# Kernel optimization log

Hardware: AMD Instinct MI355X
Metric: run time of the kernel (lower is better)

Reference implementation:

```python
import jax, jax.numpy as jnp
import numpy as np
import math

B, T, DIM = 2, 2048, 2048
N_HEADS, HEAD_DIM = 16, 128
SOFT_CAP = 30.0
EPS = 1e-6


def setup_inputs() -> dict:
    key = jax.random.key(0)
    ks = jax.random.split(key, 8)
    s = 0.02
    x = jax.random.normal(ks[0], (B, T, DIM), dtype=jnp.float32)
    # additive causal mask: 0 on/below diagonal, -1e9 above
    causal = jnp.tril(jnp.ones((T, T), dtype=bool))
    mask = jnp.where(causal, 0.0, -1e9).astype(jnp.float32)[None, None]
    Wq = jax.random.normal(ks[1], (DIM, DIM), dtype=jnp.float32) * s
    Wk = jax.random.normal(ks[2], (DIM, DIM), dtype=jnp.float32) * s
    Wv = jax.random.normal(ks[3], (DIM, DIM), dtype=jnp.float32) * s
    Wo = jax.random.normal(ks[4], (DIM, DIM), dtype=jnp.float32) * s
    ln_w = jnp.ones((DIM,), dtype=jnp.float32)
    gate_W = jax.random.normal(ks[5], (DIM, DIM), dtype=jnp.float32) * s
    gate_b = jnp.zeros((DIM,), dtype=jnp.float32)
    return {"x": x, "mask": mask, "Wq": Wq, "Wk": Wk, "Wv": Wv,
            "Wo": Wo, "ln_w": ln_w, "gate_W": gate_W, "gate_b": gate_b}


def reference(x, mask, Wq, Wk, Wv, Wo, ln_w, gate_W, gate_b):
    residual = x
    # RMSNorm
    xn = x * jax.lax.rsqrt(jnp.mean(x * x, axis=-1, keepdims=True) + EPS) * ln_w
    # projections (torch Linear: y = x @ W.T)
    q = (xn @ Wq.T).reshape(B, T, N_HEADS, HEAD_DIM)
    k = (xn @ Wk.T).reshape(B, T, N_HEADS, HEAD_DIM)
    v = (xn @ Wv.T).reshape(B, T, N_HEADS, HEAD_DIM)
    scale = 1.0 / math.sqrt(HEAD_DIM)
    logits = jnp.einsum('bqhd,bkhd->bhqk', q, k) * scale
    logits = SOFT_CAP * jnp.tanh(logits / SOFT_CAP)
    logits = logits + mask
    probs = jax.nn.softmax(logits, axis=-1)
    out = jnp.einsum('bhqk,bkhd->bqhd', probs, v).reshape(B, T, DIM)
    out = out @ Wo.T
    alpha = jax.nn.sigmoid(residual @ gate_W.T + gate_b)
    return (1.0 - alpha) * residual + alpha * out
```

## Files before the change

kernel.cpp:

```cpp
#include <hip/hip_runtime.h>
#include <hip/hip_bf16.h>
#include <cstdint>
#include <cstddef>

typedef __bf16 v8bf __attribute__((ext_vector_type(8)));
typedef float  v4f  __attribute__((ext_vector_type(4)));

using bf16 = __hip_bfloat16;

constexpr int Bdim  = 2;
constexpr int Tdim  = 2048;
constexpr int DIM   = 2048;
constexpr int NH    = 16;
constexpr int HD    = 128;
constexpr int Mrows = Bdim * Tdim;
constexpr size_t NEL  = (size_t)Mrows * DIM;
constexpr size_t W_EL = (size_t)DIM * DIM;

enum { MODE_PLAIN = 0, MODE_QK = 1, MODE_VT = 2, MODE_FINAL = 3 };

__device__ __forceinline__ float bf2f(bf16 v) { return __bfloat162float(v); }
__device__ __forceinline__ bf16  f2bf(float v) { return __float2bfloat16(v); }

__device__ __forceinline__ v8bf load8(const bf16* p) {
    return *reinterpret_cast<const v8bf*>(p);
}
__device__ __forceinline__ v8bf load8(const float* p) {
    const float4 a = *reinterpret_cast<const float4*>(p);
    const float4 b = *reinterpret_cast<const float4*>(p + 4);
    v8bf r;
    r[0] = (__bf16)a.x; r[1] = (__bf16)a.y; r[2] = (__bf16)a.z; r[3] = (__bf16)a.w;
    r[4] = (__bf16)b.x; r[5] = (__bf16)b.y; r[6] = (__bf16)b.z; r[7] = (__bf16)b.w;
    return r;
}

__device__ __forceinline__ void gll16(const void* g, void* l) {
    __builtin_amdgcn_global_load_lds(
        (__attribute__((address_space(1))) void*)g,
        (__attribute__((address_space(3))) void*)l, 16, 0, 0);
}

__global__ __launch_bounds__(256) void rms_xn_kernel(const float* __restrict__ x,
                                                     const float* __restrict__ lnw,
                                                     bf16* __restrict__ xn) {
    const int row  = blockIdx.x;
    const int base = threadIdx.x * 8;
    const float* xr = x + (size_t)row * DIM;

    const float4 a = *reinterpret_cast<const float4*>(xr + base);
    const float4 b = *reinterpret_cast<const float4*>(xr + base + 4);
    float ss = a.x*a.x + a.y*a.y + a.z*a.z + a.w*a.w
             + b.x*b.x + b.y*b.y + b.z*b.z + b.w*b.w;
#pragma unroll
    for (int off = 32; off >= 1; off >>= 1) ss += __shfl_xor(ss, off);

    __shared__ float red[4];
    const int wave = threadIdx.x >> 6;
    if ((threadIdx.x & 63) == 0) red[wave] = ss;
    __syncthreads();
    const float s = rsqrtf((red[0] + red[1] + red[2] + red[3]) * (1.0f / DIM) + 1e-6f);

    const float4 la = *reinterpret_cast<const float4*>(lnw + base);
    const float4 lb = *reinterpret_cast<const float4*>(lnw + base + 4);
    v8bf o;
    o[0] = (__bf16)(a.x * s * la.x); o[1] = (__bf16)(a.y * s * la.y);
    o[2] = (__bf16)(a.z * s * la.z); o[3] = (__bf16)(a.w * s * la.w);
    o[4] = (__bf16)(b.x * s * lb.x); o[5] = (__bf16)(b.y * s * lb.y);
    o[6] = (__bf16)(b.z * s * lb.z); o[7] = (__bf16)(b.w * s * lb.w);
    *reinterpret_cast<v8bf*>(xn + (size_t)row * DIM + base) = o;
}

__global__ __launch_bounds__(256) void conv_bf16_kernel(const float* __restrict__ s0,
                                                        const float* __restrict__ s1,
                                                        bf16* __restrict__ d0,
                                                        bf16* __restrict__ d1) {
    const int t = blockIdx.x >> 11;
    const float* s = t ? s1 : s0;
    bf16* d = t ? d1 : d0;
    const size_t i = (((size_t)(blockIdx.x & 2047)) * 256 + threadIdx.x) * 8;
    *reinterpret_cast<v8bf*>(d + i) = load8(s + i);
}

__global__ __launch_bounds__(256) void gemm_bt(
        const bf16* __restrict__ X0, const bf16* __restrict__ W0, bf16* __restrict__ Y0, int m0,
        const bf16* __restrict__ X1, const bf16* __restrict__ W1, bf16* __restrict__ Y1, int m1,
        const bf16* __restrict__ X2, const bf16* __restrict__ W2, bf16* __restrict__ Y2, int m2,
        float* __restrict__ Yf, const bf16* __restrict__ O2,
        const float* __restrict__ XR, const float* __restrict__ bias) {
    constexpr int BM = 128, BK = 32;
    __shared__ __align__(16) bf16 As[BM * BK];
    __shared__ __align__(16) bf16 Bs[BM * BK];

    const int sel = blockIdx.x >> 4;
    const bf16* X; const bf16* W; bf16* Y; int mode;
    if (sel == 0)      { X = X0; W = W0; Y = Y0; mode = m0; }
    else if (sel == 1) { X = X1; W = W1; Y = Y1; mode = m1; }
    else               { X = X2; W = W2; Y = Y2; mode = m2; }

    const int bm   = blockIdx.y * BM;
    const int bn   = (blockIdx.x & 15) * 128;
    const int tid  = threadIdx.x;
    const int lane = tid & 63;
    const int wave = tid >> 6;
    const int wm   = (wave >> 1) * 64;
    const int wn   = (wave & 1) * 64;
    const int lr   = lane & 15;
    const int lq   = lane >> 4;

    const int sr0 = tid >> 2;
    const int sc0 = (tid & 3) * 8;
    bf16* const a_l0 = As + (size_t)(wave * 64) * 8;
    bf16* const a_l1 = As + (size_t)(wave * 64 + 256) * 8;
    bf16* const b_l0 = Bs + (size_t)(wave * 64) * 8;
    bf16* const b_l1 = Bs + (size_t)(wave * 64 + 256) * 8;

    const bf16* xp0 = X + (size_t)(bm + sr0) * DIM + sc0;
    const bf16* xp1 = X + (size_t)(bm + sr0 + 64) * DIM + sc0;
    const bf16* wp0 = W + (size_t)(bn + sr0) * DIM + sc0;
    const bf16* wp1 = W + (size_t)(bn + sr0 + 64) * DIM + sc0;

    v4f acc[4][4] = {};

    for (int k0 = 0; k0 < DIM; k0 += BK) {
        gll16(xp0 + k0, a_l0);
        gll16(xp1 + k0, a_l1);
        gll16(wp0 + k0, b_l0);
        gll16(wp1 + k0, b_l1);
        __syncthreads();

        v8bf af[4], bfr[4];
#pragma unroll
        for (int i = 0; i < 4; i++) {
            af[i]  = *reinterpret_cast<const v8bf*>(&As[(wm + i * 16 + lr) * BK + lq * 8]);
            bfr[i] = *reinterpret_cast<const v8bf*>(&Bs[(wn + i * 16 + lr) * BK + lq * 8]);
        }
#pragma unroll
        for (int mi = 0; mi < 4; mi++)
#pragma unroll
            for (int ni = 0; ni < 4; ni++)
                acc[mi][ni] = __builtin_amdgcn_mfma_f32_16x16x32_bf16(af[mi], bfr[ni],
                                                                      acc[mi][ni], 0, 0, 0);
        __syncthreads();
    }

#pragma unroll
    for (int mi = 0; mi < 4; mi++) {
#pragma unroll
        for (int ni = 0; ni < 4; ni++) {
#pragma unroll
            for (int r = 0; r < 4; r++) {
                const int row = bm + wm + mi * 16 + lq * 4 + r;
                const int col = bn + wn + ni * 16 + lr;
                const float val = acc[mi][ni][r];
                if (mode == MODE_PLAIN) {
                    Y[(size_t)row * DIM + col] = f2bf(val);
                } else if (mode == MODE_QK) {
                    const int bb = row >> 11, t = row & (Tdim - 1);
                    const int hh = col >> 7, d = col & (HD - 1);
                    Y[(((size_t)(bb * NH + hh) * Tdim + t) << 7) + d] = f2bf(val);
                } else if (mode == MODE_VT) {
                    const int bb = row >> 11, t = row & (Tdim - 1);
                    const int hh = col >> 7, d = col & (HD - 1);
                    Y[(size_t)((bb * NH + hh) * HD + d) * Tdim + t] = f2bf(val);
                } else {
                    const float g  = val + bias[col];
                    const float a  = 1.0f / (1.0f + __expf(-g));
                    const size_t p = (size_t)row * DIM + col;
                    const float xv = XR[p];
                    const float ov = bf2f(O2[p]);
                    Yf[p] = xv + a * (ov - xv);
                }
            }
        }
    }
}

__global__ __launch_bounds__(256) void attn_kernel(const bf16* __restrict__ q,
                                                   const bf16* __restrict__ k,
                                                   const bf16* __restrict__ vT,
                                                   bf16* __restrict__ out) {
    __shared__ __align__(16) bf16 Ks[2][64 * 128];
    __shared__ __align__(16) bf16 Vs[2][128 * 64];
    __shared__ __align__(16) bf16 P[4][16][64];

    const int id   = blockIdx.x;
    const int seq  = id >> 3;
    const int bh   = (id & 7) + 8 * (seq >> 4);
    const int tp   = seq & 15;
    const int b    = bh >> 4;
    const int h    = bh & 15;
    const int tid  = threadIdx.x;
    const int wave = tid >> 6;
    const int lane = tid & 63;
    const int lr   = lane & 15;
    const int lq   = lane >> 4;

    const bf16* qh = q  + (size_t)bh * Tdim * HD;
    const bf16* kh = k  + (size_t)bh * Tdim * HD;
    const bf16* vh = vT + (size_t)bh * HD * Tdim;

    const bf16* ksrc[4]; const bf16* vsrc[4]; int slds[4];
#pragma unroll
    for (int i = 0; i < 4; i++) {
        const int idx = tid + i * 256;
        const int kr = idx >> 4;
        ksrc[i] = kh + (size_t)kr * HD + (((idx & 15) ^ (kr & 7)) << 3);
        const int vr = idx >> 3;
        vsrc[i] = vh + (size_t)vr * Tdim + (((idx & 7) ^ (vr & 7)) << 3);
        slds[i] = (i * 256 + wave * 64) * 8;
    }

    constexpr float C1 = 0.005892556509887896f;
    bf16 (*Pw)[64] = P[wave];

    for (int half = 0; half < 2; half++) {
        const int tile = half ? (31 - tp) : tp;
        const int q0   = tile * 64 + wave * 16;
        const int nsteps = tile + 1;

        v8bf qf[4];
#pragma unroll
        for (int c = 0; c < 4; c++)
            qf[c] = *reinterpret_cast<const v8bf*>(
                &qh[(size_t)(q0 + lr) * HD + c * 32 + lq * 8]);

        v4f oacc[8] = {};
        float psum[4] = {0.f, 0.f, 0.f, 0.f};

#pragma unroll
        for (int i = 0; i < 4; i++) gll16(ksrc[i], &Ks[0][slds[i]]);
#pragma unroll
        for (int i = 0; i < 4; i++) gll16(vsrc[i], &Vs[0][slds[i]]);
        __syncthreads();

        for (int ks = 0; ks < nsteps; ks++) {
            const int k0  = ks << 6;
            const int cur = ks & 1;

            if (ks + 1 < nsteps) {
                const size_t ko = (size_t)(k0 + 64) * HD;
                const int     vo = k0 + 64;
#pragma unroll
                for (int i = 0; i < 4; i++) gll16(ksrc[i] + ko, &Ks[cur ^ 1][slds[i]]);
#pragma unroll
                for (int i = 0; i < 4; i++) gll16(vsrc[i] + vo, &Vs[cur ^ 1][slds[i]]);
            }

            v4f sacc[4] = {};
            const char* kbase = (const char*)&Ks[cur][0];
            __builtin_amdgcn_s_setprio(1);
#pragma unroll
            for (int st = 0; st < 4; st++) {
                const int krow = st * 16 + lr;
#pragma unroll
                for (int c = 0; c < 4; c++) {
                    v8bf kf = *reinterpret_cast<const v8bf*>(
                        kbase + krow * 256 + ((((c << 2) + lq) ^ (lr & 7)) << 4));
                    sacc[st] = __builtin_amdgcn_mfma_f32_16x16x32_bf16(qf[c], kf, sacc[st], 0, 0, 0);
                }
            }
            __builtin_amdgcn_s_setprio(0);

#pragma unroll
            for (int st = 0; st < 4; st++) {
                const int kk = k0 + st * 16 + lr;
#pragma unroll
                for (int r = 0; r < 4; r++) {
                    const int qrow = q0 + lq * 4 + r;
                    const float e2 = __expf(sacc[st][r] * C1);
                    float p = __expf(-60.0f * __builtin_amdgcn_rcpf(e2 + 1.0f));
                    p = (kk > qrow) ? 0.0f : p;
                    psum[r] += p;
                    const int row = lq * 4 + r;
                    char* pb = (char*)(&Pw[row][0]);
                    const int cb = ((kk - k0) * 2) ^ ((row & 7) << 4);
                    *reinterpret_cast<bf16*>(pb + cb) = f2bf(p);
                }
            }

            asm volatile("s_waitcnt lgkmcnt(0)" ::: "memory");
            const char* prd = (const char*)(&Pw[lr][0]);
            v8bf pf0 = *reinterpret_cast<const v8bf*>(prd + ((lq * 16) ^ ((lr & 7) << 4)));
            v8bf pf1 = *reinterpret_cast<const v8bf*>(prd + ((64 + lq * 16) ^ ((lr & 7) << 4)));

            const char* vbase = (const char*)&Vs[cur][0];
            __builtin_amdgcn_s_setprio(1);
#pragma unroll
            for (int nt = 0; nt < 8; nt++) {
                const int vrow = nt * 16 + lr;
                v8bf vf0 = *reinterpret_cast<const v8bf*>(
                    vbase + vrow * 128 + (((lq)     ^ (lr & 7)) << 4));
                v8bf vf1 = *reinterpret_cast<const v8bf*>(
                    vbase + vrow * 128 + (((4 + lq) ^ (lr & 7)) << 4));
                oacc[nt] = __builtin_amdgcn_mfma_f32_16x16x32_bf16(pf0, vf0, oacc[nt], 0, 0, 0);
                oacc[nt] = __builtin_amdgcn_mfma_f32_16x16x32_bf16(pf1, vf1, oacc[nt], 0, 0, 0);
            }
            __builtin_amdgcn_s_setprio(0);

            __syncthreads();
        }

#pragma unroll
        for (int r = 0; r < 4; r++) {
#pragma unroll
            for (int off = 1; off < 16; off <<= 1) psum[r] += __shfl_xor(psum[r], off);
        }

#pragma unroll
        for (int r = 0; r < 4; r++) {
            const float inv = 1.0f / psum[r];
            const int qrow  = q0 + lq * 4 + r;
#pragma unroll
            for (int nt = 0; nt < 8; nt++) {
                out[((size_t)(b * Tdim + qrow)) * DIM + h * HD + nt * 16 + lr] =
                    f2bf(oacc[nt][r] * inv);
            }
        }
    }
}

extern "C" void kernel_launch(void* const* d_in, const int* in_sizes, int n_in,
                              void* d_out, int out_size, void* d_ws, size_t ws_size,
                              hipStream_t stream) {
    (void)out_size; (void)ws_size;
    const float* x = nullptr;
    const float* big[8] = {};
    const float* sml[4] = {};
    int nbig = 0, nsml = 0;
    for (int i = 0; i < n_in; i++) {
        if (in_sizes[i] == (int)NEL) { if (!x) x = (const float*)d_in[i]; }
        else if (in_sizes[i] == (int)W_EL) { if (nbig < 8) big[nbig++] = (const float*)d_in[i]; }
        else if (in_sizes[i] == DIM) { if (nsml < 4) sml[nsml++] = (const float*)d_in[i]; }
    }
    const int off = (nbig >= 6) ? 1 : 0;
    const float* Wq  = big[off + 0];
    const float* Wk  = big[off + 1];
    const float* Wv  = big[off + 2];
    const float* Wo  = big[off + 3];
    const float* gW  = big[off + 4];
    const float* lnw = sml[0];
    const float* gb  = sml[1];
    float* outp = (float*)d_out;

    bf16* qb  = (bf16*)d_out;
    bf16* xnb = (bf16*)d_out + NEL;
    bf16* kb  = (bf16*)((char*)d_ws + 65536);
    bf16* vb  = kb + NEL;
    bf16* mb  = (bf16*)big[0];
    bf16* ob  = kb;

    rms_xn_kernel<<<Mrows, 256, 0, stream>>>(x, lnw, xnb);
    conv_bf16_kernel<<<4096, 256, 0, stream>>>(Wq, Wk, mb, mb + W_EL);

    dim3 g16(16, 32), g32(32, 32);
    gemm_bt<<<g32, 256, 0, stream>>>(xnb, mb,        qb, MODE_QK,
                                     xnb, mb + W_EL, kb, MODE_QK,
                                     nullptr, nullptr, nullptr, 0,
                                     nullptr, nullptr, nullptr, nullptr);
    conv_bf16_kernel<<<2048, 256, 0, stream>>>(Wv, nullptr, mb, nullptr);
    gemm_bt<<<g16, 256, 0, stream>>>(xnb, mb, vb, MODE_VT,
                                     nullptr, nullptr, nullptr, 0,
                                     nullptr, nullptr, nullptr, 0,
                                     nullptr, nullptr, nullptr, nullptr);

    attn_kernel<<<512, 256, 0, stream>>>(qb, kb, vb, mb);

    conv_bf16_kernel<<<4096, 256, 0, stream>>>(Wo, gW, vb, vb + W_EL);
    gemm_bt<<<g16, 256, 0, stream>>>(mb, vb, ob, MODE_PLAIN,
                                     nullptr, nullptr, nullptr, 0,
                                     nullptr, nullptr, nullptr, 0,
                                     nullptr, nullptr, nullptr, nullptr);
    conv_bf16_kernel<<<4096, 256, 0, stream>>>(x, x + W_EL, mb, mb + W_EL);
    gemm_bt<<<g16, 256, 0, stream>>>(mb, vb + W_EL, nullptr, MODE_FINAL,
                                     nullptr, nullptr, nullptr, 0,
                                     nullptr, nullptr, nullptr, 0,
                                     outp, ob, x, gb);
}
```

Before: 534.5 us.

## Use 256x256 multistage pipelined GEMM and batch Wo/gate GEMMs with separate blend

Replaces the 128x128 single-buffered GEMM with a 512-thread 256x256 tile kernel. It uses a 4-slot LDS ring with global_load_lds prefetch three tiles ahead, XOR-swizzled LDS chunks, and setprio around the MFMA blocks. The output projection and the gate projection now run in one launch, with the gate GEMM writing a bf16 sigmoid and a separate elementwise kernel doing the residual blend. The aim is more reuse per loaded tile, hidden load latency and fewer launches. The cost is extra traffic for the bf16 sigmoid intermediate and heavier per-block register and LDS use.

```diff
diff --git a/kernel.cpp b/kernel.cpp
--- a/kernel.cpp
+++ b/kernel.cpp
@@ -17,7 +17,7 @@
 constexpr size_t NEL  = (size_t)Mrows * DIM;
 constexpr size_t W_EL = (size_t)DIM * DIM;
 
-enum { MODE_PLAIN = 0, MODE_QK = 1, MODE_VT = 2, MODE_FINAL = 3 };
+enum { MODE_PLAIN = 0, MODE_QK = 1, MODE_VT = 2, MODE_SIG = 3 };
 
 __device__ __forceinline__ float bf2f(bf16 v) { return __bfloat162float(v); }
 __device__ __forceinline__ bf16  f2bf(float v) { return __float2bfloat16(v); }
@@ -81,76 +81,132 @@
     *reinterpret_cast<v8bf*>(d + i) = load8(s + i);
 }
 
-__global__ __launch_bounds__(256) void gemm_bt(
+__global__ __launch_bounds__(256) void blend_kernel(const float* __restrict__ x,
+                                                    const bf16* __restrict__ o,
+                                                    const bf16* __restrict__ g,
+                                                    float* __restrict__ out) {
+    const size_t i = (((size_t)blockIdx.x) * 256 + threadIdx.x) * 8;
+    const v8bf ov = load8(o + i);
+    const v8bf gv = load8(g + i);
+    const float4 a = *reinterpret_cast<const float4*>(x + i);
+    const float4 b = *reinterpret_cast<const float4*>(x + i + 4);
+    float4 r0, r1;
+    r0.x = a.x + (float)gv[0] * ((float)ov[0] - a.x);
+    r0.y = a.y + (float)gv[1] * ((float)ov[1] - a.y);
+    r0.z = a.z + (float)gv[2] * ((float)ov[2] - a.z);
+    r0.w = a.w + (float)gv[3] * ((float)ov[3] - a.w);
+    r1.x = b.x + (float)gv[4] * ((float)ov[4] - b.x);
+    r1.y = b.y + (float)gv[5] * ((float)ov[5] - b.y);
+    r1.z = b.z + (float)gv[6] * ((float)ov[6] - b.z);
+    r1.w = b.w + (float)gv[7] * ((float)ov[7] - b.w);
+    *reinterpret_cast<float4*>(out + i)     = r0;
+    *reinterpret_cast<float4*>(out + i + 4) = r1;
+}
+
+__global__ __launch_bounds__(512, 2) void gemm256(
         const bf16* __restrict__ X0, const bf16* __restrict__ W0, bf16* __restrict__ Y0, int m0,
         const bf16* __restrict__ X1, const bf16* __restrict__ W1, bf16* __restrict__ Y1, int m1,
-        const bf16* __restrict__ X2, const bf16* __restrict__ W2, bf16* __restrict__ Y2, int m2,
-        float* __restrict__ Yf, const bf16* __restrict__ O2,
-        const float* __restrict__ XR, const float* __restrict__ bias) {
-    constexpr int BM = 128, BK = 32;
-    __shared__ __align__(16) bf16 As[BM * BK];
-    __shared__ __align__(16) bf16 Bs[BM * BK];
-
-    const int sel = blockIdx.x >> 4;
-    const bf16* X; const bf16* W; bf16* Y; int mode;
-    if (sel == 0)      { X = X0; W = W0; Y = Y0; mode = m0; }
-    else if (sel == 1) { X = X1; W = W1; Y = Y1; mode = m1; }
-    else               { X = X2; W = W2; Y = Y2; mode = m2; }
-
-    const int bm   = blockIdx.y * BM;
-    const int bn   = (blockIdx.x & 15) * 128;
+        const float* __restrict__ bias) {
+    constexpr int BK = 32, NT = DIM / BK;
+    __shared__ __align__(16) bf16 S[4][2][256 * BK];
+
+    const int sel = blockIdx.x >> 3;
+    const bf16* X = sel ? X1 : X0;
+    const bf16* W = sel ? W1 : W0;
+    bf16* Y       = sel ? Y1 : Y0;
+    const int mode = sel ? m1 : m0;
+
+    const int bm   = blockIdx.y * 256;
+    const int bn   = (blockIdx.x & 7) * 256;
     const int tid  = threadIdx.x;
+    const int wave = tid >> 6;
     const int lane = tid & 63;
-    const int wave = tid >> 6;
-    const int wm   = (wave >> 1) * 64;
-    const int wn   = (wave & 1) * 64;
     const int lr   = lane & 15;
     const int lq   = lane >> 4;
-
-    const int sr0 = tid >> 2;
-    const int sc0 = (tid & 3) * 8;
-    bf16* const a_l0 = As + (size_t)(wave * 64) * 8;
-    bf16* const a_l1 = As + (size_t)(wave * 64 + 256) * 8;
-    bf16* const b_l0 = Bs + (size_t)(wave * 64) * 8;
-    bf16* const b_l1 = Bs + (size_t)(wave * 64 + 256) * 8;
-
-    const bf16* xp0 = X + (size_t)(bm + sr0) * DIM + sc0;
-    const bf16* xp1 = X + (size_t)(bm + sr0 + 64) * DIM + sc0;
-    const bf16* wp0 = W + (size_t)(bn + sr0) * DIM + sc0;
-    const bf16* wp1 = W + (size_t)(bn + sr0 + 64) * DIM + sc0;
-
-    v4f acc[4][4] = {};
-
-    for (int k0 = 0; k0 < DIM; k0 += BK) {
-        gll16(xp0 + k0, a_l0);
-        gll16(xp1 + k0, a_l1);
-        gll16(wp0 + k0, b_l0);
-        gll16(wp1 + k0, b_l1);
-        __syncthreads();
-
-        v8bf af[4], bfr[4];
-#pragma unroll
-        for (int i = 0; i < 4; i++) {
-            af[i]  = *reinterpret_cast<const v8bf*>(&As[(wm + i * 16 + lr) * BK + lq * 8]);
-            bfr[i] = *reinterpret_cast<const v8bf*>(&Bs[(wn + i * 16 + lr) * BK + lq * 8]);
-        }
+    const int wr   = wave >> 2;
+    const int wc   = wave & 3;
+
+    const int c1  = tid + 512;
+    const int ar0 = tid >> 2, ar1 = c1 >> 2;
+    const int ac0 = ((tid & 3) ^ ((ar0 >> 1) & 3)) * 8;
+    const int ac1 = ((c1 & 3) ^ ((ar1 >> 1) & 3)) * 8;
+    const bf16* xs0 = X + (size_t)(bm + ar0) * DIM + ac0;
+    const bf16* xs1 = X + (size_t)(bm + ar1) * DIM + ac1;
+    const bf16* wsp0 = W + (size_t)(bn + ar0) * DIM + ac0;
+    const bf16* wsp1 = W + (size_t)(bn + ar1) * DIM + ac1;
+    const int dA0 = (wave * 64) * 8;
+    const int dA1 = (512 + wave * 64) * 8;
+
+    v4f acc[8][4] = {};
+    const int achnk = (lq ^ ((lr >> 1) & 3)) * 16;
+
+#pragma unroll
+    for (int p = 0; p < 3; p++) {
+        const size_t ko = (size_t)p * BK;
+        gll16(xs0 + ko, &S[p][0][dA0]);
+        gll16(xs1 + ko, &S[p][0][dA1]);
+        gll16(wsp0 + ko, &S[p][1][dA0]);
+        gll16(wsp1 + ko, &S[p][1][dA1]);
+    }
+
+    for (int t = 0; t < NT; ++t) {
+        if (t < NT - 2)       asm volatile("s_waitcnt vmcnt(8)" ::: "memory");
+        else if (t == NT - 2) asm volatile("s_waitcnt vmcnt(4)" ::: "memory");
+        else                  asm volatile("s_waitcnt vmcnt(0)" ::: "memory");
+        __builtin_amdgcn_sched_barrier(0);
+        __builtin_amdgcn_s_barrier();
+        __builtin_amdgcn_sched_barrier(0);
+        asm volatile("" ::: "memory");
+
+        const int slot = t & 3;
+        const char* aS = (const char*)&S[slot][0][0];
+        const char* bS = (const char*)&S[slot][1][0];
+        const bool pf  = (t + 3) < NT;
+        const int  ns  = (t + 3) & 3;
+        const size_t ko = (size_t)(t + 3) * BK;
+
+        v8bf aF[4], bF[4];
 #pragma unroll
         for (int mi = 0; mi < 4; mi++)
+            aF[mi] = *reinterpret_cast<const v8bf*>(
+                aS + (wr * 128 + mi * 16 + lr) * 64 + achnk);
+#pragma unroll
+        for (int ni = 0; ni < 4; ni++)
+            bF[ni] = *reinterpret_cast<const v8bf*>(
+                bS + (wc * 64 + ni * 16 + lr) * 64 + achnk);
+        if (pf) { gll16(xs0 + ko, &S[ns][0][dA0]); gll16(xs1 + ko, &S[ns][0][dA1]); }
+        __builtin_amdgcn_s_setprio(1);
+#pragma unroll
+        for (int mi = 0; mi < 4; mi++)
 #pragma unroll
             for (int ni = 0; ni < 4; ni++)
-                acc[mi][ni] = __builtin_amdgcn_mfma_f32_16x16x32_bf16(af[mi], bfr[ni],
-                                                                      acc[mi][ni], 0, 0, 0);
-        __syncthreads();
-    }
-
-#pragma unroll
-    for (int mi = 0; mi < 4; mi++) {
+                acc[mi][ni] = __builtin_amdgcn_mfma_f32_16x16x32_bf16(
+                    aF[mi], bF[ni], acc[mi][ni], 0, 0, 0);
+        __builtin_amdgcn_s_setprio(0);
+
+#pragma unroll
+        for (int mi = 0; mi < 4; mi++)
+            aF[mi] = *reinterpret_cast<const v8bf*>(
+                aS + (wr * 128 + (mi + 4) * 16 + lr) * 64 + achnk);
+        if (pf) { gll16(wsp0 + ko, &S[ns][1][dA0]); gll16(wsp1 + ko, &S[ns][1][dA1]); }
+        __builtin_amdgcn_s_setprio(1);
+#pragma unroll
+        for (int mi = 0; mi < 4; mi++)
+#pragma unroll
+            for (int ni = 0; ni < 4; ni++)
+                acc[mi + 4][ni] = __builtin_amdgcn_mfma_f32_16x16x32_bf16(
+                    aF[mi], bF[ni], acc[mi + 4][ni], 0, 0, 0);
+        __builtin_amdgcn_s_setprio(0);
+    }
+
+#pragma unroll
+    for (int mi = 0; mi < 8; mi++) {
 #pragma unroll
         for (int ni = 0; ni < 4; ni++) {
 #pragma unroll
             for (int r = 0; r < 4; r++) {
-                const int row = bm + wm + mi * 16 + lq * 4 + r;
-                const int col = bn + wn + ni * 16 + lr;
+                const int row = bm + wr * 128 + mi * 16 + lq * 4 + r;
+                const int col = bn + wc * 64 + ni * 16 + lr;
                 const float val = acc[mi][ni][r];
                 if (mode == MODE_PLAIN) {
                     Y[(size_t)row * DIM + col] = f2bf(val);
@@ -163,12 +219,8 @@
                     const int hh = col >> 7, d = col & (HD - 1);
                     Y[(size_t)((bb * NH + hh) * HD + d) * Tdim + t] = f2bf(val);
                 } else {
-                    const float g  = val + bias[col];
-                    const float a  = 1.0f / (1.0f + __expf(-g));
-                    const size_t p = (size_t)row * DIM + col;
-                    const float xv = XR[p];
-                    const float ov = bf2f(O2[p]);
-                    Yf[p] = xv + a * (ov - xv);
+                    const float g = val + bias[col];
+                    Y[(size_t)row * DIM + col] = f2bf(1.0f / (1.0f + __expf(-g)));
                 }
             }
         }
@@ -348,31 +400,28 @@
     bf16* vb  = kb + NEL;
     bf16* mb  = (bf16*)big[0];
     bf16* ob  = kb;
+    bf16* sig = vb;
+    bf16* wob = (bf16*)d_out;
+    bf16* gwb = wob + W_EL;
+    bf16* xbf = (bf16*)d_out + NEL;
 
     rms_xn_kernel<<<Mrows, 256, 0, stream>>>(x, lnw, xnb);
     conv_bf16_kernel<<<4096, 256, 0, stream>>>(Wq, Wk, mb, mb + W_EL);
 
-    dim3 g16(16, 32), g32(32, 32);
-    gemm_bt<<<g32, 256, 0, stream>>>(xnb, mb,        qb, MODE_QK,
-                                     xnb, mb + W_EL, kb, MODE_QK,
-                                     nullptr, nullptr, nullptr, 0,
-                                     nullptr, nullptr, nullptr, nullptr);
+    dim3 gqk(16, 16), gv(8, 16);
+    gemm256<<<gqk, 512, 0, stream>>>(xnb, mb,        qb, MODE_QK,
+                                     xnb, mb + W_EL, kb, MODE_QK, nullptr);
     conv_bf16_kernel<<<2048, 256, 0, stream>>>(Wv, nullptr, mb, nullptr);
-    gemm_bt<<<g16, 256, 0, stream>>>(xnb, mb, vb, MODE_VT,
-                                     nullptr, nullptr, nullptr, 0,
-                                     nullptr, nullptr, nullptr, 0,
-                                     nullptr, nullptr, nullptr, nullptr);
+    gemm256<<<gv, 512, 0, stream>>>(xnb, mb, vb, MODE_VT,
+                                    nullptr, nullptr, nullptr, 0, nullptr);
 
     attn_kernel<<<512, 256, 0, stream>>>(qb, kb, vb, mb);
 
-    conv_bf16_kernel<<<4096, 256, 0, stream>>>(Wo, gW, vb, vb + W_EL);
-    gemm_bt<<<g16, 256, 0, stream>>>(mb, vb, ob, MODE_PLAIN,
-                                     nullptr, nullptr, nullptr, 0,
-                                     nullptr, nullptr, nullptr, 0,
-                                     nullptr, nullptr, nullptr, nullptr);
-    conv_bf16_kernel<<<4096, 256, 0, stream>>>(x, x + W_EL, mb, mb + W_EL);
-    gemm_bt<<<g16, 256, 0, stream>>>(mb, vb + W_EL, nullptr, MODE_FINAL,
-                                     nullptr, nullptr, nullptr, 0,
-                                     nullptr, nullptr, nullptr, 0,
-                                     outp, ob, x, gb);
-}
+    conv_bf16_kernel<<<4096, 256, 0, stream>>>(Wo, gW, wob, gwb);
+    conv_bf16_kernel<<<4096, 256, 0, stream>>>(x, x + W_EL, xbf, xbf + W_EL);
+
+    gemm256<<<gqk, 512, 0, stream>>>(mb,  wob, ob,  MODE_PLAIN,
+                                     xbf, gwb, sig, MODE_SIG, gb);
+
+    blend_kernel<<<4096, 256, 0, stream>>>(x, ob, sig, outp);
+}
```

Measured after the change: 502.8 us. 5.9% less time.
